# Optimization experiments

Measured on AMD Instinct MI355X. Metric: run time of the kernel, lower is better.

Reference implementation:

```python
import jax, jax.numpy as jnp
import numpy as np

N = 20000      # n_nodes
E = 320000     # n_edges (multiple of 4, so _from_coo drops nothing)
D = 512        # embed_dim
H = 8          # num_heads
DK = D // H    # d_k = 64


def setup_inputs() -> dict:
    key = jax.random.key(0)
    ks = jax.random.split(key, 12)
    x = jax.random.normal(ks[0], (N, D), jnp.float32)
    rows = jnp.sort(jax.random.randint(ks[1], (E,), 0, N))
    cols = jax.random.randint(ks[2], (E,), 0, N)
    edge_index = jnp.stack([rows, cols]).astype(jnp.int32)  # [2, E]
    att_bias = jax.random.normal(ks[3], (E, H), jnp.float32)
    s = float(1.0 / np.sqrt(D))  # ~xavier scale
    Wq = jax.random.normal(ks[4], (D, D), jnp.float32) * s
    Wk = jax.random.normal(ks[5], (D, D), jnp.float32) * s
    Wv = jax.random.normal(ks[6], (D, D), jnp.float32) * s
    Wo = jax.random.normal(ks[7], (D, D), jnp.float32) * s
    bq = jnp.zeros((D,), jnp.float32)
    bk = jnp.zeros((D,), jnp.float32)
    bv = jnp.zeros((D,), jnp.float32)
    bo = jnp.zeros((D,), jnp.float32)
    return dict(x=x, edge_index=edge_index, att_bias=att_bias,
                Wq=Wq, bq=bq, Wk=Wk, bk=bk, Wv=Wv, bv=bv, Wo=Wo, bo=bo)


def reference(x, edge_index, att_bias, Wq, bq, Wk, bk, Wv, bv, Wo, bo):
    n = x.shape[0]
    rows, cols = edge_index[0], edge_index[1]
    # per-head projections: [n, H, DK]
    q = (x @ Wq + bq).reshape(n, H, DK)
    k = (x @ Wk + bk).reshape(n, H, DK)
    v = (x @ Wv + bv).reshape(n, H, DK)
    scale = 1.0 / jnp.sqrt(jnp.asarray(DK, x.dtype))
    # masked QK^T on the edge pattern, plus additive bias: [E, H]
    logits = jnp.einsum('ehd,ehd->eh', q[rows] * scale, k[cols]) + att_bias
    # CSR (segment) softmax over each destination row
    row_max = jax.ops.segment_max(logits, rows, num_segments=n)      # [n, H]
    p = jnp.exp(logits - row_max[rows])                              # [E, H]
    denom = jax.ops.segment_sum(p, rows, num_segments=n)            # [n, H]
    att = p / denom[rows]                                            # [E, H]
    # sparse-dense bmm: y[i] = sum_{e: rows[e]=i} att[e] * v[cols[e]]
    y = jax.ops.segment_sum(att[:, :, None] * v[cols], rows, num_segments=n)  # [n, H, DK]
    out = y.reshape(n, H * DK) @ Wo + bo
    return out
```

## Files before the change

### kernel.cpp

```cpp
#include <hip/hip_runtime.h>
#include <hip/hip_bf16.h>

typedef unsigned short ushort_t;
typedef unsigned int uint32;
typedef __attribute__((ext_vector_type(8))) short short8;
typedef __attribute__((ext_vector_type(4))) float floatx4;

#define DEV __device__ __forceinline__

#if defined(__has_builtin)
#if __has_builtin(__builtin_amdgcn_sdot4)
#define HAS_SDOT 1
#endif
#endif
#ifndef HAS_SDOT
#define HAS_SDOT 0
#endif

DEV float b2f(ushort_t u) { return __uint_as_float(((uint32)u) << 16); }
DEV ushort_t f2b(float f) {
  __hip_bfloat16 h = __float2bfloat16(f);
  return __builtin_bit_cast(unsigned short, h);
}
DEV void unpack8(const uint4& u, float* f) {
  f[0] = __uint_as_float(u.x << 16); f[1] = __uint_as_float(u.x & 0xffff0000u);
  f[2] = __uint_as_float(u.y << 16); f[3] = __uint_as_float(u.y & 0xffff0000u);
  f[4] = __uint_as_float(u.z << 16); f[5] = __uint_as_float(u.z & 0xffff0000u);
  f[6] = __uint_as_float(u.w << 16); f[7] = __uint_as_float(u.w & 0xffff0000u);
}
DEV void unpack_i8x8(uint2 u, float* f) {
  f[0] = (float)((int)(u.x << 24) >> 24);
  f[1] = (float)((int)(u.x << 16) >> 24);
  f[2] = (float)((int)(u.x << 8) >> 24);
  f[3] = (float)((int)u.x >> 24);
  f[4] = (float)((int)(u.y << 24) >> 24);
  f[5] = (float)((int)(u.y << 16) >> 24);
  f[6] = (float)((int)(u.y << 8) >> 24);
  f[7] = (float)((int)u.y >> 24);
}

#define GLOAD_LDS(gp, lp) \
  __builtin_amdgcn_global_load_lds((const __attribute__((address_space(1))) uint32*)(gp), \
                                   (__attribute__((address_space(3))) uint32*)(lp), 16, 0, 0)

#define KVROW 1088

DEV int xcd_swz(int wg, int nwg) {
  int q = nwg >> 3, r = nwg & 7;
  int xcd = wg & 7, idx = wg >> 3;
  return (xcd < r ? xcd * (q + 1) : r * (q + 1) + (xcd - r) * q) + idx;
}

__global__ __launch_bounds__(256) void k_prep(
    const void* __restrict__ x,
    const void* __restrict__ Wq, const void* __restrict__ Wk,
    const void* __restrict__ Wv, const void* __restrict__ Wo,
    ushort_t* __restrict__ WT4,
    const void* __restrict__ bq, const void* __restrict__ bk,
    const void* __restrict__ bv, const void* __restrict__ bo,
    float* __restrict__ biasf, ushort_t* __restrict__ xb,
    const void* __restrict__ ab, float* __restrict__ ABc,
    const int* __restrict__ rows, int* __restrict__ rp, int* __restrict__ flag,
    int E, int Nn, int n8, int n4, int abEarly,
    int oRp, int oAb) {
  __shared__ int red[256];
  __shared__ ushort_t t[32][33];
  int b = blockIdx.x;
  int tid = threadIdx.x;

  if (b >= oRp && b < oAb) {
    int i = (b - oRp) * 256 + tid;
    if (i > Nn) return;
    int lo = 0, hi = E;
    while (lo < hi) {
      int mid = (lo + hi) >> 1;
      if (rows[mid] < i) lo = mid + 1; else hi = mid;
    }
    rp[i] = lo;
    return;
  }

  const ushort_t* xs = (const ushort_t*)x;
  int wild = 0;
  for (int i = tid; i < 4096; i += 256) {
    uint32 e = (xs[i] >> 7) & 0xFFu;
    if (e < 100u || e > 140u) wild++;
  }
  red[tid] = wild;
  __syncthreads();
  for (int s = 128; s > 0; s >>= 1) {
    if (tid < s) red[tid] += red[tid + s];
    __syncthreads();
  }
  int isf32 = red[0] > 400;

  if (b < 1024) {
    int z = b >> 8, rem = b & 255;
    int by = rem >> 4, bx = rem & 15;
    int tx = tid & 31, ty = tid >> 5;
    const void* src = (z == 0) ? Wq : (z == 1) ? Wk : (z == 2) ? Wv : Wo;
    ushort_t* dst = WT4 + (size_t)z * 512 * 512;
#pragma unroll
    for (int i = 0; i < 4; i++) {
      size_t idx = (size_t)(by * 32 + ty + 8 * i) * 512 + bx * 32 + tx;
      ushort_t v = isf32 ? f2b(((const float*)src)[idx]) : ((const ushort_t*)src)[idx];
      t[ty + 8 * i][tx] = v;
    }
    __syncthreads();
#pragma unroll
    for (int i = 0; i < 4; i++)
      dst[(size_t)(bx * 32 + ty + 8 * i) * 512 + by * 32 + tx] = t[tx][ty + 8 * i];
  } else if (b < 1032) {
    if (b == 1024 && tid == 0) flag[0] = isf32;
    int i = (b - 1024) * 256 + tid;
    if (i >= 2048) return;
    int z = i >> 9, j = i & 511;
    const void* bb = (z == 0) ? bq : (z == 1) ? bk : (z == 2) ? bv : bo;
    biasf[i] = isf32 ? ((const float*)bb)[j] : b2f(((const ushort_t*)bb)[j]);
  } else if (b < oRp) {
    int i = (b - 1032) * 256 + tid;
    if (i >= n8) return;
    if (isf32) {
      const float* xf = (const float*)x + (size_t)i * 8;
      float4 f0 = ((const float4*)xf)[0];
      float4 f1 = ((const float4*)xf)[1];
      uint4 o;
      o.x = (uint32)f2b(f0.x) | ((uint32)f2b(f0.y) << 16);
      o.y = (uint32)f2b(f0.z) | ((uint32)f2b(f0.w) << 16);
      o.z = (uint32)f2b(f1.x) | ((uint32)f2b(f1.y) << 16);
      o.w = (uint32)f2b(f1.z) | ((uint32)f2b(f1.w) << 16);
      ((uint4*)xb)[i] = o;
    } else {
      ((uint4*)xb)[i] = ((const uint4*)x)[i];
    }
  } else {
    if (!abEarly || isf32) return;
    int i = (b - oAb) * 256 + tid;
    if (i >= n4) return;
    uint2 u = ((const uint2*)ab)[i];
    float4 o;
    o.x = __uint_as_float(u.x << 16);
    o.y = __uint_as_float(u.x & 0xffff0000u);
    o.z = __uint_as_float(u.y << 16);
    o.w = __uint_as_float(u.y & 0xffff0000u);
    ((float4*)ABc)[i] = o;
  }
}

__global__ __launch_bounds__(256) void k_convab(
    const void* __restrict__ ab, float* __restrict__ ABc, int n4,
    const int* __restrict__ flagp) {
  if (*flagp) return;
  int i = blockIdx.x * 256 + threadIdx.x;
  if (i >= n4) return;
  uint2 u = ((const uint2*)ab)[i];
  float4 o;
  o.x = __uint_as_float(u.x << 16);
  o.y = __uint_as_float(u.x & 0xffff0000u);
  o.z = __uint_as_float(u.y << 16);
  o.w = __uint_as_float(u.y & 0xffff0000u);
  ((float4*)ABc)[i] = o;
}

DEV void gemm_body256(const ushort_t* __restrict__ A, const ushort_t* __restrict__ BT,
                      const float* __restrict__ bias, void* C,
                      int M, int ldc, float scale, int row0, int by, int mode) {
  __shared__ ushort_t Ab[2][256 * 64];
  __shared__ ushort_t Bb[2][256 * 64];
  int tid = threadIdx.x;
  int w = tid >> 6, lane = tid & 63;
  int lm = lane & 15, quad = lane >> 4;
  int wr = w >> 2, wc = w & 3;

  asm volatile("s_waitcnt vmcnt(0)" ::: "memory");

  int clog8 = ((lane & 7) ^ (lane >> 3)) * 8;
  int arow[4], brow[4];
#pragma unroll
  for (int i = 0; i < 4; i++) {
    int r = row0 + i * 64 + w * 8 + (lane >> 3);
    arow[i] = (r < M) ? r : (M - 1);
    brow[i] = by * 256 + i * 64 + w * 8 + (lane >> 3);
  }

  floatx4 acc[8][4];
#pragma unroll
  for (int i = 0; i < 8; i++)
#pragma unroll
    for (int j = 0; j < 4; j++)
#pragma unroll
      for (int r = 0; r < 4; r++) acc[i][j][r] = 0.f;

  auto stage = [&](int buf, int kt) {
    int k0 = kt * 64 + clog8;
#pragma unroll
    for (int i = 0; i < 4; i++)
      GLOAD_LDS(A + (size_t)arow[i] * 512 + k0, &Ab[buf][(i * 64 + w * 8) * 64]);
#pragma unroll
    for (int i = 0; i < 4; i++)
      GLOAD_LDS(BT + (size_t)brow[i] * 512 + k0, &Bb[buf][(i * 64 + w * 8) * 64]);
  };

  int ph0 = ((0 + quad) ^ (lm & 7)) * 8;
  int ph1 = ((4 + quad) ^ (lm & 7)) * 8;

  auto compute = [&](int cur) {
#pragma unroll
    for (int kk = 0; kk < 2; kk++) {
      int ph = kk ? ph1 : ph0;
      const ushort_t* pa = &Ab[cur][(wr * 128 + lm) * 64] + ph;
      const ushort_t* pb = &Bb[cur][(wc * 64 + lm) * 64] + ph;
      short8 af[8], bf[4];
#pragma unroll
      for (int nt = 0; nt < 4; nt++) bf[nt] = *(const short8*)(pb + nt * 16 * 64);
#pragma unroll
      for (int mt = 0; mt < 8; mt++) af[mt] = *(const short8*)(pa + mt * 16 * 64);
      __builtin_amdgcn_s_setprio(1);
#pragma unroll
      for (int mt = 0; mt < 8; mt++)
#pragma unroll
        for (int nt = 0; nt < 4; nt++)
          acc[mt][nt] = __builtin_amdgcn_mfma_f32_16x16x32_bf16(af[mt], bf[nt], acc[mt][nt], 0, 0, 0);
      __builtin_amdgcn_s_setprio(0);
    }
  };

  stage(0, 0);
#pragma unroll 1
  for (int kt = 0; kt < 8; ++kt) {
    int cur = kt & 1;
    if (kt < 7) {
      stage(cur ^ 1, kt + 1);
      asm volatile("s_waitcnt vmcnt(8)" ::: "memory");
    } else {
      asm volatile("s_waitcnt vmcnt(0)" ::: "memory");
    }
    __builtin_amdgcn_s_barrier();
    compute(cur);
    if (kt < 7) {
      asm volatile("s_waitcnt lgkmcnt(0)" ::: "memory");
      __builtin_amdgcn_s_barrier();
    }
  }

  int colB = by * 256 + wc * 64 + lm;
  float bv4[4];
#pragma unroll
  for (int nt = 0; nt < 4; nt++) bv4[nt] = bias[colB + nt * 16];

  if (mode <= 1) {
#pragma unroll
    for (int mt = 0; mt < 8; mt++) {
      int rg0 = row0 + wr * 128 + mt * 16 + quad * 4;
#pragma unroll
      for (int nt = 0; nt < 4; nt++) {
#pragma unroll
        for (int r = 0; r < 4; r++) {
          int rg = rg0 + r;
          if (rg < M) {
            float val = (acc[mt][nt][r] + bv4[nt]) * scale;
            size_t off = (size_t)rg * ldc + colB + nt * 16;
            if (mode == 1) ((float*)C)[off] = val;
            else           ((ushort_t*)C)[off] = f2b(val);
          }
        }
      }
    }
  } else {
    int vslot = (mode == 4);
    int head = (by * 256 + wc * 64) >> 6;
#pragma unroll
    for (int mt = 0; mt < 8; mt++) {
#pragma unroll
      for (int r = 0; r < 4; r++) {
        int rg = row0 + wr * 128 + mt * 16 + quad * 4 + r;
        float v0 = acc[mt][0][r] + bv4[0];
        float v1 = acc[mt][1][r] + bv4[1];
        float v2 = acc[mt][2][r] + bv4[2];
        float v3 = acc[mt][3][r] + bv4[3];
        float am = fmaxf(fmaxf(fabsf(v0), fabsf(v1)), fmaxf(fabsf(v2), fabsf(v3)));
        am = fmaxf(am, __shfl_xor(am, 1));
        am = fmaxf(am, __shfl_xor(am, 2));
        am = fmaxf(am, __shfl_xor(am, 4));
        am = fmaxf(am, __shfl_xor(am, 8));
        am = fmaxf(am, 1e-20f);
        float inv8 = 127.0f / am;
        float sc8 = am * (1.0f / 127.0f);
        if (rg < M) {
          unsigned char* Crow = (unsigned char*)C + (size_t)rg * KVROW;
          unsigned char* bp = Crow + head * 128 + (lm >> 3) * 16 + 8 * vslot + (lm & 7);
          bp[ 0] = (unsigned char)(signed char)(int)rintf(v0 * inv8);
          bp[32] = (unsigned char)(signed char)(int)rintf(v1 * inv8);
          bp[64] = (unsigned char)(signed char)(int)rintf(v2 * inv8);
          bp[96] = (unsigned char)(signed char)(int)rintf(v3 * inv8);
          if (lm == 0)
            *(float*)(Crow + 1024 + head * 8 + vslot * 4) = sc8;
        }
      }
    }
  }
}

__global__ __launch_bounds__(512, 2) void k_gemm_qkv(
    const ushort_t* __restrict__ xb, const ushort_t* __restrict__ WT4,
    const float* __restrict__ biasf, ushort_t* Qp, unsigned char* KV8, int M) {
  int swz = xcd_swz(blockIdx.x, gridDim.x);
  int row = swz / 6;
  int sub = swz - row * 6;
  int by = sub & 1, z = sub >> 1;
  const ushort_t* BT = WT4 + (size_t)z * 512 * 512;
  const float* bias = biasf + (size_t)z * 512;
  if (z == 0)
    gemm_body256(xb, BT, bias, Qp, M, 512, 0.125f, row * 256, by, 0);
  else
    gemm_body256(xb, BT, bias, KV8, M, 0, 1.0f, row * 256, by, z == 1 ? 3 : 4);
}

__global__ __launch_bounds__(512, 2) void k_gemm_out(
    const ushort_t* __restrict__ y, const ushort_t* __restrict__ WT4,
    const float* __restrict__ biasf, void* out, int M,
    const int* __restrict__ flagp) {
  int mode = *flagp;
  int swz = xcd_swz(blockIdx.x, gridDim.x);
  int row = swz >> 1, by = swz & 1;
  gemm_body256(y, WT4 + (size_t)3 * 512 * 512, biasf + 3 * 512, out, M, 512, 1.0f,
               row * 256, by, mode);
}

__global__ __launch_bounds__(256) void k_edge(
    ushort_t* Qy, const unsigned char* __restrict__ KV8,
    const void* __restrict__ ab, const float* __restrict__ ABc,
    const int* __restrict__ cols, const int* __restrict__ rp, int Nn,
    const int* __restrict__ flagp) {
  int node = blockIdx.x * 4 + (threadIdx.x >> 6);
  if (node >= Nn) return;
  int lane = threadIdx.x & 63;
  int h8 = lane >> 3;
  const float* abf32 = (*flagp) ? (const float*)ab : ABc;

  uint4 qu = ((const uint4*)(Qy + (size_t)node * 512))[lane];
  float qf[8];
  unpack8(qu, qf);

#if HAS_SDOT
  float qa = 0.f;
#pragma unroll
  for (int j = 0; j < 8; j++) qa = fmaxf(qa, fabsf(qf[j]));
  qa = fmaxf(qa, __shfl_xor(qa, 1));
  qa = fmaxf(qa, __shfl_xor(qa, 2));
  qa = fmaxf(qa, __shfl_xor(qa, 4));
  qa = fmaxf(qa, 1e-20f);
  float qs = qa * (1.0f / 127.0f);
  float qinv = 127.0f / qa;
  int qp0 = 0, qp1 = 0;
#pragma unroll
  for (int j = 0; j < 4; j++) qp0 |= (((int)rintf(qf[j] * qinv)) & 0xFF) << (8 * j);
#pragma unroll
  for (int j = 4; j < 8; j++) qp1 |= (((int)rintf(qf[j] * qinv)) & 0xFF) << (8 * (j - 4));
#endif

  int e0 = rp[node], e1 = rp[node + 1];
  int cnt = e1 - e0;

  float s0 = 0.f, s1 = 0.f;
  float acc0[8], acc1[8];
#pragma unroll
  for (int j = 0; j < 8; j++) { acc0[j] = 0.f; acc1[j] = 0.f; }

  uint4 kvb[4];
  float2 scb[4];
  float abv[4];

  for (int base = 0; base < cnt; base += 64) {
    int rem = cnt - base; if (rem > 64) rem = 64;
    int li = (lane < rem) ? lane : (rem - 1);
    int myc = cols[e0 + base + li];
    const float* abp = abf32 + (size_t)(e0 + base) * 8 + h8;

    auto pref = [&](int t, int slot) {
      int valid = t < rem;
      int c = __builtin_amdgcn_readlane(myc, valid ? t : 0);
      const unsigned char* kvrow = KV8 + (size_t)c * KVROW;
      kvb[slot] = *(const uint4*)(kvrow + lane * 16);
      scb[slot] = *(const float2*)(kvrow + 1024 + h8 * 8);
      float a = abp[(valid ? t : 0) * 8];
      abv[slot] = valid ? a : -1e30f;
    };
    auto consume = [&](int slot, float* acc, float& s) {
#if HAS_SDOT
      int di = __builtin_amdgcn_sdot4(qp0, (int)kvb[slot].x, 0, false);
      di = __builtin_amdgcn_sdot4(qp1, (int)kvb[slot].y, di, false);
      di += __shfl_xor(di, 1);
      di += __shfl_xor(di, 2);
      di += __shfl_xor(di, 4);
      float logit = fminf(fmaf((float)di * qs, scb[slot].x, abv[slot]), 80.f);
#else
      float kf[8];
      uint2 ku; ku.x = kvb[slot].x; ku.y = kvb[slot].y;
      unpack_i8x8(ku, kf);
      float d = 0.f;
#pragma unroll
      for (int j = 0; j < 8; j++) d = fmaf(qf[j], kf[j], d);
      d += __shfl_xor(d, 1);
      d += __shfl_xor(d, 2);
      d += __shfl_xor(d, 4);
      float logit = fminf(fmaf(d, scb[slot].x, abv[slot]), 80.f);
#endif
      float pw = __expf(logit);
      s += pw;
      float pwv = pw * scb[slot].y;
      float vf[8];
      uint2 vu; vu.x = kvb[slot].z; vu.y = kvb[slot].w;
      unpack_i8x8(vu, vf);
#pragma unroll
      for (int j = 0; j < 8; j++) acc[j] = fmaf(pwv, vf[j], acc[j]);
    };

    pref(0, 0); pref(1, 1); pref(2, 2); pref(3, 3);
    int iters = (rem + 3) >> 2;
    for (int it = 0; it < iters; ++it) {
      int nt = it * 4 + 4;
      consume(0, acc0, s0); pref(nt + 0, 0);
      consume(1, acc1, s1); pref(nt + 1, 1);
      consume(2, acc0, s0); pref(nt + 2, 2);
      consume(3, acc1, s1); pref(nt + 3, 3);
    }
  }

  float s = s0 + s1;
  float inv = (cnt > 0 && s > 0.f) ? 1.f / s : 0.f;
  ushort_t hb[8];
#pragma unroll
  for (int j = 0; j < 8; j++) hb[j] = f2b((acc0[j] + acc1[j]) * inv);
  uint4 uh;
  uh.x = (uint32)hb[0] | ((uint32)hb[1] << 16);
  uh.y = (uint32)hb[2] | ((uint32)hb[3] << 16);
  uh.z = (uint32)hb[4] | ((uint32)hb[5] << 16);
  uh.w = (uint32)hb[6] | ((uint32)hb[7] << 16);
  ((uint4*)(Qy + (size_t)node * 512))[lane] = uh;
}

extern "C" void kernel_launch(void* const* d_in, const int* in_sizes, int n_in,
                              void* d_out, int out_size, void* d_ws, size_t ws_size,
                              hipStream_t stream) {
  const void* x  = d_in[0];
  const int* ei  = (const int*)d_in[1];
  const void* ab = d_in[2];
  const void* Wq = d_in[3];
  const void* bq = d_in[4];
  const void* Wk = d_in[5];
  const void* bk = d_in[6];
  const void* Wv = d_in[7];
  const void* bv = d_in[8];
  const void* Wo = d_in[9];
  const void* bo = d_in[10];

  const int D = 512;
  int M = in_sizes[0] / D;
  int E = in_sizes[1] / 2;
  const int* rows = ei;
  const int* cols = ei + E;

  char* p = (char*)d_ws;
  size_t off = 0;
  auto carve = [&](size_t bytes) -> void* {
    off = (off + 255) & ~(size_t)255;
    void* r = p + off;
    off += bytes;
    return r;
  };
  int* flag          = (int*)carve(4);
  ushort_t* WT4      = (ushort_t*)carve((size_t)4 * 512 * 512 * 2);
  float* biasf       = (float*)carve((size_t)4 * 512 * 4);
  ushort_t* xb       = (ushort_t*)carve((size_t)M * 512 * 2);
  ushort_t* Qp       = (ushort_t*)carve((size_t)M * 512 * 2);
  unsigned char* KV8 = (unsigned char*)carve((size_t)M * KVROW);
  int* rp            = (int*)carve((size_t)(M + 1) * 4);

  int n4 = E * 8 / 4;
  size_t abBytes = (size_t)E * 8 * 4;
  float* ABc;
  int abEarly;
  if (off + 256 + abBytes <= ws_size) {
    ABc = (float*)carve(abBytes);
    abEarly = 1;
  } else {
    ABc = (float*)xb;
    abEarly = 0;
  }

  int n8 = M * 512 / 8;
  int nCx = (n8 + 255) / 256;
  int nRp = (M + 1 + 255) / 256;
  int nAb = (n4 + 255) / 256;
  int oRp = 1032 + nCx;
  int oAb = oRp + nRp;
  int oEnd = oAb + nAb;

  k_prep<<<oEnd, 256, 0, stream>>>(x, Wq, Wk, Wv, Wo, WT4, bq, bk, bv, bo,
                                   biasf, xb, ab, ABc, rows, rp, flag,
                                   E, M, n8, n4, abEarly, oRp, oAb);

  int rt = (M + 255) / 256;
  k_gemm_qkv<<<rt * 6, 512, 0, stream>>>(xb, WT4, biasf, Qp, KV8, M);
  if (!abEarly)
    k_convab<<<nAb, 256, 0, stream>>>(ab, ABc, n4, flag);
  k_edge<<<(M + 3) / 4, 256, 0, stream>>>(Qp, KV8, ab, ABc, cols, rp, M, flag);
  k_gemm_out<<<rt * 2, 512, 0, stream>>>(Qp, WT4, biasf, d_out, M, flag);
}
```

Baseline: 259.9 us.

## Split each node's edges across four waves and reduce partials in LDS

The edge-attention kernel now gives each node a full 256-thread block instead of one wavefront. The four waves process interleaved edges, and their partial accumulators and softmax sums are combined through shared memory before wave 0 writes the output. This adds parallelism per node, aimed at shortening the serial edge loop, which averages about 16 edges per row. The cost is four times as many blocks, a __syncthreads, and LDS reduction traffic. Waves may also idle when a row has few edges.

```diff
diff --git a/kernel.cpp b/kernel.cpp
--- a/kernel.cpp
+++ b/kernel.cpp
@@ -332,8 +332,9 @@
     const void* __restrict__ ab, const float* __restrict__ ABc,
     const int* __restrict__ cols, const int* __restrict__ rp, int Nn,
     const int* __restrict__ flagp) {
-  int node = blockIdx.x * 4 + (threadIdx.x >> 6);
-  if (node >= Nn) return;
+  __shared__ float part[3][64][10];
+  int node = blockIdx.x;
+  int w = threadIdx.x >> 6;
   int lane = threadIdx.x & 63;
   int h8 = lane >> 3;
   const float* abf32 = (*flagp) ? (const float*)ab : ABc;
@@ -416,28 +417,45 @@
       for (int j = 0; j < 8; j++) acc[j] = fmaf(pwv, vf[j], acc[j]);
     };
 
-    pref(0, 0); pref(1, 1); pref(2, 2); pref(3, 3);
-    int iters = (rem + 3) >> 2;
+    pref(w + 0, 0); pref(w + 4, 1); pref(w + 8, 2); pref(w + 12, 3);
+    int iters = (rem + 15) >> 4;
     for (int it = 0; it < iters; ++it) {
-      int nt = it * 4 + 4;
+      int nt = w + 16 * (it + 1);
       consume(0, acc0, s0); pref(nt + 0, 0);
-      consume(1, acc1, s1); pref(nt + 1, 1);
-      consume(2, acc0, s0); pref(nt + 2, 2);
-      consume(3, acc1, s1); pref(nt + 3, 3);
-    }
-  }
-
-  float s = s0 + s1;
-  float inv = (cnt > 0 && s > 0.f) ? 1.f / s : 0.f;
-  ushort_t hb[8];
-#pragma unroll
-  for (int j = 0; j < 8; j++) hb[j] = f2b((acc0[j] + acc1[j]) * inv);
-  uint4 uh;
-  uh.x = (uint32)hb[0] | ((uint32)hb[1] << 16);
-  uh.y = (uint32)hb[2] | ((uint32)hb[3] << 16);
-  uh.z = (uint32)hb[4] | ((uint32)hb[5] << 16);
-  uh.w = (uint32)hb[6] | ((uint32)hb[7] << 16);
-  ((uint4*)(Qy + (size_t)node * 512))[lane] = uh;
+      consume(1, acc1, s1); pref(nt + 4, 1);
+      consume(2, acc0, s0); pref(nt + 8, 2);
+      consume(3, acc1, s1); pref(nt + 12, 3);
+    }
+  }
+
+  if (w > 0) {
+#pragma unroll
+    for (int j = 0; j < 8; j++) part[w - 1][lane][j] = acc0[j] + acc1[j];
+    part[w - 1][lane][8] = s0 + s1;
+  }
+  __syncthreads();
+  if (w == 0) {
+    float accT[8];
+    float s = s0 + s1;
+#pragma unroll
+    for (int j = 0; j < 8; j++) accT[j] = acc0[j] + acc1[j];
+#pragma unroll
+    for (int p = 0; p < 3; p++) {
+#pragma unroll
+      for (int j = 0; j < 8; j++) accT[j] += part[p][lane][j];
+      s += part[p][lane][8];
+    }
+    float inv = (cnt > 0 && s > 0.f) ? 1.f / s : 0.f;
+    ushort_t hb[8];
+#pragma unroll
+    for (int j = 0; j < 8; j++) hb[j] = f2b(accT[j] * inv);
+    uint4 uh;
+    uh.x = (uint32)hb[0] | ((uint32)hb[1] << 16);
+    uh.y = (uint32)hb[2] | ((uint32)hb[3] << 16);
+    uh.z = (uint32)hb[4] | ((uint32)hb[5] << 16);
+    uh.w = (uint32)hb[6] | ((uint32)hb[7] << 16);
+    ((uint4*)(Qy + (size_t)node * 512))[lane] = uh;
+  }
 }
 
 extern "C" void kernel_launch(void* const* d_in, const int* in_sizes, int n_in,
@@ -505,6 +523,6 @@
   k_gemm_qkv<<<rt * 6, 512, 0, stream>>>(xb, WT4, biasf, Qp, KV8, M);
   if (!abEarly)
     k_convab<<<nAb, 256, 0, stream>>>(ab, ABc, n4, flag);
-  k_edge<<<(M + 3) / 4, 256, 0, stream>>>(Qp, KV8, ab, ABc, cols, rp, M, flag);
+  k_edge<<<M, 256, 0, stream>>>(Qp, KV8, ab, ABc, cols, rp, M, flag);
   k_gemm_out<<<rt * 2, 512, 0, stream>>>(Qp, WT4, biasf, d_out, M, flag);
 }
```

Measured after the change: 296.3 us. 14.0% more time.
